# Kernel tuning notes

Measured on AMD Instinct MI355X. Metric: run time of the kernel, lower is better.

Reference implementation:

```python
import jax, jax.numpy as jnp
import numpy as np

B, L, H, NH = 4, 1024, 768, 12
HS = H // NH          # 64
DPB_DIM = H // 4      # 192
TEMPERATURE = 1.0


def setup_inputs() -> dict:
    key = jax.random.key(0)
    ks = jax.random.split(key, 10)
    def xavier(k, shape):
        fan_in, fan_out = shape[0], shape[-1]
        std = (2.0 / (fan_in + fan_out)) ** 0.5
        return jax.random.normal(k, shape, dtype=jnp.float32) * std
    return {
        "x": jax.random.normal(ks[0], (B, L, H), dtype=jnp.float32),
        "adj": jax.random.normal(ks[1], (B, 1, L, L), dtype=jnp.float32),
        "mask": jnp.ones((B, L), dtype=bool),
        "weights": xavier(ks[2], (H, 3 * H)),
        "in_bias": jnp.zeros((1, 1, 3 * H), dtype=jnp.float32),
        "out_bias": jnp.zeros((1, 1, H), dtype=jnp.float32),
        "dpb_w0": xavier(ks[3], (1, DPB_DIM)),
        "dpb_b0": jnp.zeros((DPB_DIM,), dtype=jnp.float32),
        "dpb_w1": xavier(ks[4], (DPB_DIM, DPB_DIM)),
        "dpb_b1": jnp.zeros((DPB_DIM,), dtype=jnp.float32),
        "dpb_w2": xavier(ks[5], (DPB_DIM, NH)),
        "dpb_b2": jnp.zeros((NH,), dtype=jnp.float32),
    }


def _dyn_pos_bias(n, w0, b0, w1, b1, w2, b2):
    # relative positions -(n-1)..(n-1) -> per-head bias [NH, n, n]
    pos = jnp.arange(-n + 1, n, dtype=jnp.float32)[:, None]      # [2n-1, 1]
    hdn = jax.nn.silu(pos @ w0 + b0)
    hdn = jax.nn.silu(hdn @ w1 + b1)
    table = hdn @ w2 + b2                                        # [2n-1, NH]
    idx = jnp.arange(n)[:, None] - jnp.arange(n)[None, :] + (n - 1)  # [n, n]
    return jnp.transpose(table[idx], (2, 0, 1))                  # [NH, n, n]


def reference(x, adj, mask, weights, in_bias, out_bias,
              dpb_w0, dpb_b0, dpb_w1, dpb_b1, dpb_w2, dpb_b2):
    b, l, h = x.shape
    qkv = x @ weights + in_bias                                  # [b, l, 3h]
    # view(b,l,NH,-1).permute(0,2,1,3).chunk(3, dim=3): split 3*HS per head
    qkv = jnp.transpose(qkv.reshape(b, l, NH, 3 * HS), (0, 2, 1, 3))  # [b,NH,l,3HS]
    Q, K, V = qkv[..., :HS], qkv[..., HS:2 * HS], qkv[..., 2 * HS:]
    norm = HS ** 0.5
    attention = jnp.einsum('bhid,bhjd->bhij', Q, K) / TEMPERATURE / norm
    raw_attention = attention                                    # returned pre-bias
    attn_bias = _dyn_pos_bias(l, dpb_w0, dpb_b0, dpb_w1, dpb_b1, dpb_w2, dpb_b2)
    attention = attention + attn_bias[None] + adj
    mask_value = -jnp.finfo(attention.dtype).max
    attention = jnp.where(mask[:, None, None, :], attention, mask_value)
    attention = jax.nn.softmax(attention, axis=-1)
    out = attention @ V                                          # [b,NH,l,HS]
    out = jnp.transpose(out, (0, 2, 1, 3)).reshape(b, l, h)
    out = out + out_bias
    return (out, raw_attention)
```

## Files before the change

kernel.cpp:

```cpp
#include <hip/hip_runtime.h>
#include <stdint.h>
#include <stddef.h>


#define BB 4
#define LL 1024
#define NHH 12
#define HSS 64
#define HH 768
#define OUT_ELEMS (BB * LL * HH)
#define QKV_ELEMS (BB * NHH * LL * HSS)

typedef __attribute__((ext_vector_type(8))) short short8;
typedef __attribute__((ext_vector_type(4))) float f32x4;

__device__ __forceinline__ float bf2f(ushort u) {
    union { unsigned int i; float f; } v; v.i = ((unsigned int)u) << 16; return v.f;
}
__device__ __forceinline__ ushort f2bf(float f) {
    union { float f; unsigned int i; } v; v.f = f;
    unsigned int r = v.i + 0x7FFFu + ((v.i >> 16) & 1u);
    return (ushort)(r >> 16);
}

__global__ void sentinel_kernel(float* out) {
    if (threadIdx.x == 0) out[0] = 12345.0f;
}

__global__ void dpb_kernel(const float* __restrict__ w0, const float* __restrict__ b0,
                           const float* __restrict__ w1, const float* __restrict__ b1,
                           const float* __restrict__ w2, const float* __restrict__ b2,
                           float* __restrict__ table) {
    __shared__ float h0s[192];
    __shared__ float h1s[192];
    int r = blockIdx.x, j = threadIdx.x;
    double pos = (double)(r - 1023);
    double a = pos * (double)w0[j] + (double)b0[j];
    h0s[j] = (float)(a / (1.0 + exp(-a)));
    __syncthreads();
    double acc = (double)b1[j];
    for (int k = 0; k < 192; ++k) acc += (double)h0s[k] * (double)w1[k * 192 + j];
    h1s[j] = (float)(acc / (1.0 + exp(-acc)));
    __syncthreads();
    if (j < 12) {
        double t = (double)b2[j];
        for (int k = 0; k < 192; ++k) t += (double)h1s[k] * (double)w2[k * 12 + j];
        table[r * 12 + j] = (float)t;
    }
}

__global__ __launch_bounds__(256)
void qkv_mfma(const float* __restrict__ x, const float* __restrict__ w,
              const float* __restrict__ bias,
              ushort* __restrict__ Qb, ushort* __restrict__ Kb, ushort* __restrict__ Vb) {
    __shared__ ushort As[64][32];
    __shared__ ushort Bts[64][56];

    int m0 = blockIdx.y * 64, n0 = blockIdx.x * 64;
    int tid = threadIdx.x, lane = tid & 63, wid = tid >> 6;
    int wr = wid >> 1, wc = wid & 1;
    int g = lane >> 4, qi = lane & 15;
    f32x4 acc[2][2] = {};

    int arow = tid >> 2, acol = (tid & 3) * 8;
    int bn = tid & 63, bkb = (tid >> 6) * 8;

    for (int k0 = 0; k0 < 768; k0 += 32) {
        float4 a0 = *(const float4*)(x + (size_t)(m0 + arow) * 768 + k0 + acol);
        float4 a1 = *(const float4*)(x + (size_t)(m0 + arow) * 768 + k0 + acol + 4);
        float bt[8];
        #pragma unroll
        for (int i = 0; i < 8; ++i)
            bt[i] = w[(size_t)(k0 + bkb + i) * 2304 + n0 + bn];
        short8 av, bv;
        av[0] = (short)f2bf(a0.x); av[1] = (short)f2bf(a0.y);
        av[2] = (short)f2bf(a0.z); av[3] = (short)f2bf(a0.w);
        av[4] = (short)f2bf(a1.x); av[5] = (short)f2bf(a1.y);
        av[6] = (short)f2bf(a1.z); av[7] = (short)f2bf(a1.w);
        #pragma unroll
        for (int i = 0; i < 8; ++i) bv[i] = (short)f2bf(bt[i]);
        *(short8*)&As[arow][acol] = av;
        *(short8*)&Bts[bn][bkb] = bv;
        __syncthreads();

        short8 af0 = *(const short8*)&As[wr * 32 + qi][g * 8];
        short8 af1 = *(const short8*)&As[wr * 32 + 16 + qi][g * 8];
        short8 bf0 = *(const short8*)&Bts[wc * 32 + qi][g * 8];
        short8 bf1 = *(const short8*)&Bts[wc * 32 + 16 + qi][g * 8];
        acc[0][0] = __builtin_amdgcn_mfma_f32_16x16x32_bf16(af0, bf0, acc[0][0], 0, 0, 0);
        acc[0][1] = __builtin_amdgcn_mfma_f32_16x16x32_bf16(af0, bf1, acc[0][1], 0, 0, 0);
        acc[1][0] = __builtin_amdgcn_mfma_f32_16x16x32_bf16(af1, bf0, acc[1][0], 0, 0, 0);
        acc[1][1] = __builtin_amdgcn_mfma_f32_16x16x32_bf16(af1, bf1, acc[1][1], 0, 0, 0);
        __syncthreads();
    }

    #pragma unroll
    for (int ti = 0; ti < 2; ++ti)
    #pragma unroll
    for (int tj = 0; tj < 2; ++tj)
    #pragma unroll
    for (int r = 0; r < 4; ++r) {
        int row = m0 + wr * 32 + ti * 16 + g * 4 + r;
        int col = n0 + wc * 32 + tj * 16 + qi;
        float val = acc[ti][tj][r] + bias[col];
        int h = col / 192, rem = col % 192;
        int which = rem >> 6, d = rem & 63;
        int bb = row >> 10, ll = row & 1023;
        ushort* dst = which == 0 ? Qb : (which == 1 ? Kb : Vb);
        dst[(((size_t)(bb * 12 + h) * 1024 + ll) << 6) + d] = f2bf(val);
    }
}

__global__ __launch_bounds__(256)
void attn_mfma(const ushort* __restrict__ Qb, const ushort* __restrict__ Kb,
               const ushort* __restrict__ Vb, const float* __restrict__ adj,
               const float* __restrict__ table,
               ushort* __restrict__ Opart, float* __restrict__ MZ,
               float* __restrict__ raw) {
    __shared__ ushort Ks[64][72];
    __shared__ ushort Vt[64][72];
    __shared__ ushort Ps[4][16][72];
    __shared__ float  tbl[576];

    int blk = blockIdx.x;
    int lb = (blk & 7) * 192 + (blk >> 3);
    int bh = lb >> 5;
    int rest = lb & 31;
    int half = rest >> 4;
    int qb = rest & 15;
    int h = bh % 12;
    int b = bh / 12;
    int q0 = qb * 64;
    int j_start = half * 512;
    int tid = threadIdx.x, lane = tid & 63, wid = tid >> 6;
    int g = lane >> 4, qi = lane & 15;
    int qg = q0 + wid * 16 + qi;
    int qrel = wid * 16 + qi;

    int tbase = q0 - j_start + 512;
    for (int i = tid; i < 575; i += 256) tbl[i] = table[(tbase + i) * 12 + h];

    short8 qfrag[2];
    qfrag[0] = *(const short8*)(Qb + ((size_t)(bh * 1024 + qg) << 6) + g * 8);
    qfrag[1] = *(const short8*)(Qb + ((size_t)(bh * 1024 + qg) << 6) + 32 + g * 8);

    float m = -INFINITY, ssum = 0.f;
    f32x4 oacc[4] = {};

    int krow = tid >> 2, kcol = (tid & 3) * 16;
    int vd = tid & 63, vjb = (tid >> 6) * 16;

    short8 kr0, kr1, vr0, vr1;
    {
        const ushort* kp = Kb + ((size_t)(bh * 1024 + j_start + krow) << 6) + kcol;
        kr0 = *(const short8*)kp;
        kr1 = *(const short8*)(kp + 8);
        ushort tmp[16];
        #pragma unroll
        for (int i = 0; i < 16; ++i)
            tmp[i] = Vb[((size_t)(bh * 1024 + j_start + vjb + i) << 6) + vd];
        #pragma unroll
        for (int i = 0; i < 8; ++i) { vr0[i] = (short)tmp[i]; vr1[i] = (short)tmp[i + 8]; }
    }

    for (int it = 0; it < 8; ++it) {
        int j0 = j_start + it * 64;
        *(short8*)&Ks[krow][kcol] = kr0;
        *(short8*)&Ks[krow][kcol + 8] = kr1;
        *(short8*)&Vt[vd][vjb] = vr0;
        *(short8*)&Vt[vd][vjb + 8] = vr1;
        __syncthreads();

        if (it < 7) {
            int jn = j0 + 64;
            const ushort* kp = Kb + ((size_t)(bh * 1024 + jn + krow) << 6) + kcol;
            kr0 = *(const short8*)kp;
            kr1 = *(const short8*)(kp + 8);
            ushort tmp[16];
            #pragma unroll
            for (int i = 0; i < 16; ++i)
                tmp[i] = Vb[((size_t)(bh * 1024 + jn + vjb + i) << 6) + vd];
            #pragma unroll
            for (int i = 0; i < 8; ++i) { vr0[i] = (short)tmp[i]; vr1[i] = (short)tmp[i + 8]; }
        }

        f32x4 sacc[4];
        #pragma unroll
        for (int jt = 0; jt < 4; ++jt) {
            short8 kf0 = *(const short8*)&Ks[jt * 16 + qi][g * 8];
            short8 kf1 = *(const short8*)&Ks[jt * 16 + qi][32 + g * 8];
            f32x4 z = {0.f, 0.f, 0.f, 0.f};
            z = __builtin_amdgcn_mfma_f32_16x16x32_bf16(kf0, qfrag[0], z, 0, 0, 0);
            z = __builtin_amdgcn_mfma_f32_16x16x32_bf16(kf1, qfrag[1], z, 0, 0, 0);
            sacc[jt] = z;
        }

        float lg[16];
        #pragma unroll
        for (int jt = 0; jt < 4; ++jt) {
            int jbase = j0 + jt * 16 + g * 4;
            f32x4 sv = sacc[jt] * 0.125f;
            *(f32x4*)(raw + ((size_t)(bh * 1024 + qg) << 10) + jbase) = sv;
            float4 av = *(const float4*)(adj + ((size_t)(b * 1024 + qg) << 10) + jbase);
            int ib = qrel + j_start + 511 - jbase;
            lg[jt * 4 + 0] = sv[0] + tbl[ib] + av.x;
            lg[jt * 4 + 1] = sv[1] + tbl[ib - 1] + av.y;
            lg[jt * 4 + 2] = sv[2] + tbl[ib - 2] + av.z;
            lg[jt * 4 + 3] = sv[3] + tbl[ib - 3] + av.w;
        }

        float cmax = lg[0];
        #pragma unroll
        for (int i = 1; i < 16; ++i) cmax = fmaxf(cmax, lg[i]);
        cmax = fmaxf(cmax, __shfl_xor(cmax, 16));
        cmax = fmaxf(cmax, __shfl_xor(cmax, 32));
        float newm = fmaxf(m, cmax);
        float corr = __expf(m - newm);
        float p[16], csum = 0.f;
        #pragma unroll
        for (int i = 0; i < 16; ++i) { p[i] = __expf(lg[i] - newm); csum += p[i]; }
        csum += __shfl_xor(csum, 16);
        csum += __shfl_xor(csum, 32);
        ssum = ssum * corr + csum;
        m = newm;
        #pragma unroll
        for (int dt = 0; dt < 4; ++dt) oacc[dt] *= corr;

        #pragma unroll
        for (int jt = 0; jt < 4; ++jt) {
            ushort4 pw;
            #pragma unroll
            for (int r = 0; r < 4; ++r) ((ushort*)&pw)[r] = f2bf(p[jt * 4 + r]);
            *(ushort4*)&Ps[wid][qi][jt * 16 + g * 4] = pw;
        }
        short8 pf0 = *(const short8*)&Ps[wid][qi][g * 8];
        short8 pf1 = *(const short8*)&Ps[wid][qi][32 + g * 8];
        #pragma unroll
        for (int dt = 0; dt < 4; ++dt) {
            short8 vf0 = *(const short8*)&Vt[dt * 16 + qi][g * 8];
            short8 vf1 = *(const short8*)&Vt[dt * 16 + qi][32 + g * 8];
            oacc[dt] = __builtin_amdgcn_mfma_f32_16x16x32_bf16(vf0, pf0, oacc[dt], 0, 0, 0);
            oacc[dt] = __builtin_amdgcn_mfma_f32_16x16x32_bf16(vf1, pf1, oacc[dt], 0, 0, 0);
        }
        __syncthreads();
    }

    int pb = (bh * 16 + qb) * 2 + half;
    #pragma unroll
    for (int dt = 0; dt < 4; ++dt) {
        ushort4 ow;
        #pragma unroll
        for (int r = 0; r < 4; ++r) ((ushort*)&ow)[r] = f2bf(oacc[dt][r]);
        *(ushort4*)(Opart + (size_t)pb * 4096 + qrel * 64 + dt * 16 + g * 4) = ow;
    }
    if (g == 0) {
        MZ[pb * 128 + qrel * 2] = m;
        MZ[pb * 128 + qrel * 2 + 1] = ssum;
    }
}

__global__ __launch_bounds__(256)
void combine_kernel(const ushort* __restrict__ Opart, const float* __restrict__ MZ,
                    const float* __restrict__ out_bias, float* __restrict__ out) {
    int cb = blockIdx.x;
    int bh = cb >> 4, qb = cb & 15;
    int h = bh % 12, b = bh / 12;
    int t = threadIdx.x;
    int q = t >> 2, dg = (t & 3) * 16;
    int p0 = cb * 2, p1 = p0 + 1;
    float m0 = MZ[p0 * 128 + q * 2], Z0 = MZ[p0 * 128 + q * 2 + 1];
    float m1 = MZ[p1 * 128 + q * 2], Z1 = MZ[p1 * 128 + q * 2 + 1];
    float mm = fmaxf(m0, m1);
    float a0 = __expf(m0 - mm), a1 = __expf(m1 - mm);
    float inv = 1.f / (a0 * Z0 + a1 * Z1);
    const ushort* r0 = Opart + (size_t)p0 * 4096 + q * 64 + dg;
    const ushort* r1 = Opart + (size_t)p1 * 4096 + q * 64 + dg;
    short8 x0a = *(const short8*)r0, x0b = *(const short8*)(r0 + 8);
    short8 x1a = *(const short8*)r1, x1b = *(const short8*)(r1 + 8);
    float* op = out + (size_t)(b * 1024 + qb * 64 + q) * 768 + h * 64 + dg;
    const float* ob = out_bias + h * 64 + dg;
    float res[16];
    #pragma unroll
    for (int i = 0; i < 8; ++i) {
        res[i]     = (a0 * bf2f((ushort)x0a[i]) + a1 * bf2f((ushort)x1a[i])) * inv + ob[i];
        res[i + 8] = (a0 * bf2f((ushort)x0b[i]) + a1 * bf2f((ushort)x1b[i])) * inv + ob[i + 8];
    }
    #pragma unroll
    for (int i = 0; i < 4; ++i)
        *(float4*)(op + i * 4) = *(float4*)(res + i * 4);
}

extern "C" void kernel_launch(void* const* d_in, const int* in_sizes, int n_in,
                              void* d_out, int out_size, void* d_ws, size_t ws_size,
                              hipStream_t stream) {
    const float* x        = (const float*)d_in[0];
    const float* adj      = (const float*)d_in[1];
    const float* weights  = (const float*)d_in[3];
    const float* in_bias  = (const float*)d_in[4];
    const float* out_bias = (const float*)d_in[5];
    const float* dpb_w0   = (const float*)d_in[6];
    const float* dpb_b0   = (const float*)d_in[7];
    const float* dpb_w1   = (const float*)d_in[8];
    const float* dpb_b1   = (const float*)d_in[9];
    const float* dpb_w2   = (const float*)d_in[10];
    const float* dpb_b2   = (const float*)d_in[11];

    float* out = (float*)d_out;
    float* raw = out + OUT_ELEMS;

    float*  table = (float*)d_ws;
    ushort* Qb    = (ushort*)((char*)d_ws + 98304);
    ushort* Kb    = Qb + QKV_ELEMS;
    ushort* Vb    = Kb + QKV_ELEMS;
    ushort* Opart = Vb + QKV_ELEMS;
    float*  MZ    = (float*)(Opart + (size_t)1536 * 4096);
    size_t need = 98304 + 3 * (size_t)QKV_ELEMS * 2
                + (size_t)1536 * 4096 * 2 + (size_t)1536 * 128 * 4;
    if (ws_size < need) {
        sentinel_kernel<<<1, 64, 0, stream>>>(out);
        return;
    }

    dpb_kernel<<<2047, 192, 0, stream>>>(dpb_w0, dpb_b0, dpb_w1, dpb_b1, dpb_w2, dpb_b2, table);
    qkv_mfma<<<dim3(2304 / 64, 4096 / 64), 256, 0, stream>>>(x, weights, in_bias, Qb, Kb, Vb);
    attn_mfma<<<1536, 256, 0, stream>>>(Qb, Kb, Vb, adj, table, Opart, MZ, raw);
    combine_kernel<<<768, 256, 0, stream>>>(Opart, MZ, out_bias, out);
}
```

Baseline: 147.7 us.

## Pre-convert QKV inputs to bf16, pipeline GEMM loads, prefetch adj in attention

```diff
diff --git a/kernel.cpp b/kernel.cpp
--- a/kernel.cpp
+++ b/kernel.cpp
@@ -10,6 +10,8 @@
 #define HH 768
 #define OUT_ELEMS (BB * LL * HH)
 #define QKV_ELEMS (BB * NHH * LL * HSS)
+#define X_ELEMS (BB * LL * HH)
+#define W_ELEMS (HH * 3 * HH)
 
 typedef __attribute__((ext_vector_type(8))) short short8;
 typedef __attribute__((ext_vector_type(4))) float f32x4;
@@ -25,6 +27,20 @@
 
 __global__ void sentinel_kernel(float* out) {
     if (threadIdx.x == 0) out[0] = 12345.0f;
+}
+
+__global__ __launch_bounds__(256)
+void cvt_bf16(const float* __restrict__ src, ushort* __restrict__ dst, int n) {
+    int i = (blockIdx.x * 256 + threadIdx.x) * 8;
+    if (i >= n) return;
+    float4 a = *(const float4*)(src + i);
+    float4 b = *(const float4*)(src + i + 4);
+    short8 o;
+    o[0] = (short)f2bf(a.x); o[1] = (short)f2bf(a.y);
+    o[2] = (short)f2bf(a.z); o[3] = (short)f2bf(a.w);
+    o[4] = (short)f2bf(b.x); o[5] = (short)f2bf(b.y);
+    o[6] = (short)f2bf(b.z); o[7] = (short)f2bf(b.w);
+    *(short8*)(dst + i) = o;
 }
 
 __global__ void dpb_kernel(const float* __restrict__ w0, const float* __restrict__ b0,
@@ -50,11 +66,11 @@
 }
 
 __global__ __launch_bounds__(256)
-void qkv_mfma(const float* __restrict__ x, const float* __restrict__ w,
+void qkv_mfma(const ushort* __restrict__ x, const ushort* __restrict__ w,
               const float* __restrict__ bias,
               ushort* __restrict__ Qb, ushort* __restrict__ Kb, ushort* __restrict__ Vb) {
-    __shared__ ushort As[64][32];
-    __shared__ ushort Bts[64][56];
+    __shared__ ushort As[64][72];
+    __shared__ ushort Bts[64][72];
 
     int m0 = blockIdx.y * 64, n0 = blockIdx.x * 64;
     int tid = threadIdx.x, lane = tid & 63, wid = tid >> 6;
@@ -62,35 +78,55 @@
     int g = lane >> 4, qi = lane & 15;
     f32x4 acc[2][2] = {};
 
-    int arow = tid >> 2, acol = (tid & 3) * 8;
-    int bn = tid & 63, bkb = (tid >> 6) * 8;
-
-    for (int k0 = 0; k0 < 768; k0 += 32) {
-        float4 a0 = *(const float4*)(x + (size_t)(m0 + arow) * 768 + k0 + acol);
-        float4 a1 = *(const float4*)(x + (size_t)(m0 + arow) * 768 + k0 + acol + 4);
-        float bt[8];
-        #pragma unroll
-        for (int i = 0; i < 8; ++i)
-            bt[i] = w[(size_t)(k0 + bkb + i) * 2304 + n0 + bn];
-        short8 av, bv;
-        av[0] = (short)f2bf(a0.x); av[1] = (short)f2bf(a0.y);
-        av[2] = (short)f2bf(a0.z); av[3] = (short)f2bf(a0.w);
-        av[4] = (short)f2bf(a1.x); av[5] = (short)f2bf(a1.y);
-        av[6] = (short)f2bf(a1.z); av[7] = (short)f2bf(a1.w);
-        #pragma unroll
-        for (int i = 0; i < 8; ++i) bv[i] = (short)f2bf(bt[i]);
-        *(short8*)&As[arow][acol] = av;
-        *(short8*)&Bts[bn][bkb] = bv;
+    int arow = tid >> 2, acol = (tid & 3) * 16;
+    int bn = tid & 63, bkb = (tid >> 6) * 16;
+
+    const size_t xrow = (size_t)(m0 + arow) * 768;
+    short8 ar0, ar1, br0, br1;
+
+    {
+        ar0 = *(const short8*)(x + xrow + acol);
+        ar1 = *(const short8*)(x + xrow + acol + 8);
+        ushort t[16];
+        #pragma unroll
+        for (int i = 0; i < 16; ++i)
+            t[i] = w[(size_t)(bkb + i) * 2304 + n0 + bn];
+        #pragma unroll
+        for (int i = 0; i < 8; ++i) { br0[i] = (short)t[i]; br1[i] = (short)t[i + 8]; }
+    }
+
+    for (int kt = 0; kt < 12; ++kt) {
+        *(short8*)&As[arow][acol] = ar0;
+        *(short8*)&As[arow][acol + 8] = ar1;
+        *(short8*)&Bts[bn][bkb] = br0;
+        *(short8*)&Bts[bn][bkb + 8] = br1;
         __syncthreads();
 
-        short8 af0 = *(const short8*)&As[wr * 32 + qi][g * 8];
-        short8 af1 = *(const short8*)&As[wr * 32 + 16 + qi][g * 8];
-        short8 bf0 = *(const short8*)&Bts[wc * 32 + qi][g * 8];
-        short8 bf1 = *(const short8*)&Bts[wc * 32 + 16 + qi][g * 8];
-        acc[0][0] = __builtin_amdgcn_mfma_f32_16x16x32_bf16(af0, bf0, acc[0][0], 0, 0, 0);
-        acc[0][1] = __builtin_amdgcn_mfma_f32_16x16x32_bf16(af0, bf1, acc[0][1], 0, 0, 0);
-        acc[1][0] = __builtin_amdgcn_mfma_f32_16x16x32_bf16(af1, bf0, acc[1][0], 0, 0, 0);
-        acc[1][1] = __builtin_amdgcn_mfma_f32_16x16x32_bf16(af1, bf1, acc[1][1], 0, 0, 0);
+        if (kt < 11) {
+            int k0 = kt * 64 + 64;
+            ar0 = *(const short8*)(x + xrow + k0 + acol);
+            ar1 = *(const short8*)(x + xrow + k0 + acol + 8);
+            ushort t[16];
+            #pragma unroll
+            for (int i = 0; i < 16; ++i)
+                t[i] = w[(size_t)(k0 + bkb + i) * 2304 + n0 + bn];
+            #pragma unroll
+            for (int i = 0; i < 8; ++i) { br0[i] = (short)t[i]; br1[i] = (short)t[i + 8]; }
+        }
+
+        __builtin_amdgcn_s_setprio(1);
+        #pragma unroll
+        for (int kk = 0; kk < 64; kk += 32) {
+            short8 af0 = *(const short8*)&As[wr * 32 + qi][kk + g * 8];
+            short8 af1 = *(const short8*)&As[wr * 32 + 16 + qi][kk + g * 8];
+            short8 bf0 = *(const short8*)&Bts[wc * 32 + qi][kk + g * 8];
+            short8 bf1 = *(const short8*)&Bts[wc * 32 + 16 + qi][kk + g * 8];
+            acc[0][0] = __builtin_amdgcn_mfma_f32_16x16x32_bf16(af0, bf0, acc[0][0], 0, 0, 0);
+            acc[0][1] = __builtin_amdgcn_mfma_f32_16x16x32_bf16(af0, bf1, acc[0][1], 0, 0, 0);
+            acc[1][0] = __builtin_amdgcn_mfma_f32_16x16x32_bf16(af1, bf0, acc[1][0], 0, 0, 0);
+            acc[1][1] = __builtin_amdgcn_mfma_f32_16x16x32_bf16(af1, bf1, acc[1][1], 0, 0, 0);
+        }
+        __builtin_amdgcn_s_setprio(0);
         __syncthreads();
     }
 
@@ -111,7 +147,7 @@
     }
 }
 
-__global__ __launch_bounds__(256)
+__global__ __launch_bounds__(256, 5)
 void attn_mfma(const ushort* __restrict__ Qb, const ushort* __restrict__ Kb,
                const ushort* __restrict__ Vb, const float* __restrict__ adj,
                const float* __restrict__ table,
@@ -150,7 +186,10 @@
     int krow = tid >> 2, kcol = (tid & 3) * 16;
     int vd = tid & 63, vjb = (tid >> 6) * 16;
 
+    const float* adjrow = adj + ((size_t)(b * 1024 + qg) << 10);
+
     short8 kr0, kr1, vr0, vr1;
+    float4 acur[4], anxt[4];
     {
         const ushort* kp = Kb + ((size_t)(bh * 1024 + j_start + krow) << 6) + kcol;
         kr0 = *(const short8*)kp;
@@ -161,6 +200,9 @@
             tmp[i] = Vb[((size_t)(bh * 1024 + j_start + vjb + i) << 6) + vd];
         #pragma unroll
         for (int i = 0; i < 8; ++i) { vr0[i] = (short)tmp[i]; vr1[i] = (short)tmp[i + 8]; }
+        #pragma unroll
+        for (int jt = 0; jt < 4; ++jt)
+            acur[jt] = *(const float4*)(adjrow + j_start + jt * 16 + g * 4);
     }
 
     for (int it = 0; it < 8; ++it) {
@@ -182,9 +224,13 @@
                 tmp[i] = Vb[((size_t)(bh * 1024 + jn + vjb + i) << 6) + vd];
             #pragma unroll
             for (int i = 0; i < 8; ++i) { vr0[i] = (short)tmp[i]; vr1[i] = (short)tmp[i + 8]; }
+            #pragma unroll
+            for (int jt = 0; jt < 4; ++jt)
+                anxt[jt] = *(const float4*)(adjrow + jn + jt * 16 + g * 4);
         }
 
         f32x4 sacc[4];
+        __builtin_amdgcn_s_setprio(1);
         #pragma unroll
         for (int jt = 0; jt < 4; ++jt) {
             short8 kf0 = *(const short8*)&Ks[jt * 16 + qi][g * 8];
@@ -194,6 +240,7 @@
             z = __builtin_amdgcn_mfma_f32_16x16x32_bf16(kf1, qfrag[1], z, 0, 0, 0);
             sacc[jt] = z;
         }
+        __builtin_amdgcn_s_setprio(0);
 
         float lg[16];
         #pragma unroll
@@ -201,12 +248,11 @@
             int jbase = j0 + jt * 16 + g * 4;
             f32x4 sv = sacc[jt] * 0.125f;
             *(f32x4*)(raw + ((size_t)(bh * 1024 + qg) << 10) + jbase) = sv;
-            float4 av = *(const float4*)(adj + ((size_t)(b * 1024 + qg) << 10) + jbase);
             int ib = qrel + j_start + 511 - jbase;
-            lg[jt * 4 + 0] = sv[0] + tbl[ib] + av.x;
-            lg[jt * 4 + 1] = sv[1] + tbl[ib - 1] + av.y;
-            lg[jt * 4 + 2] = sv[2] + tbl[ib - 2] + av.z;
-            lg[jt * 4 + 3] = sv[3] + tbl[ib - 3] + av.w;
+            lg[jt * 4 + 0] = sv[0] + tbl[ib] + acur[jt].x;
+            lg[jt * 4 + 1] = sv[1] + tbl[ib - 1] + acur[jt].y;
+            lg[jt * 4 + 2] = sv[2] + tbl[ib - 2] + acur[jt].z;
+            lg[jt * 4 + 3] = sv[3] + tbl[ib - 3] + acur[jt].w;
         }
 
         float cmax = lg[0];
@@ -235,6 +281,7 @@
         }
         short8 pf0 = *(const short8*)&Ps[wid][qi][g * 8];
         short8 pf1 = *(const short8*)&Ps[wid][qi][32 + g * 8];
+        __builtin_amdgcn_s_setprio(1);
         #pragma unroll
         for (int dt = 0; dt < 4; ++dt) {
             short8 vf0 = *(const short8*)&Vt[dt * 16 + qi][g * 8];
@@ -242,7 +289,11 @@
             oacc[dt] = __builtin_amdgcn_mfma_f32_16x16x32_bf16(vf0, pf0, oacc[dt], 0, 0, 0);
             oacc[dt] = __builtin_amdgcn_mfma_f32_16x16x32_bf16(vf1, pf1, oacc[dt], 0, 0, 0);
         }
+        __builtin_amdgcn_s_setprio(0);
         __syncthreads();
+
+        #pragma unroll
+        for (int jt = 0; jt < 4; ++jt) acur[jt] = anxt[jt];
     }
 
     int pb = (bh * 16 + qb) * 2 + half;
@@ -308,21 +359,26 @@
     float* out = (float*)d_out;
     float* raw = out + OUT_ELEMS;
 
-    float*  table = (float*)d_ws;
-    ushort* Qb    = (ushort*)((char*)d_ws + 98304);
-    ushort* Kb    = Qb + QKV_ELEMS;
-    ushort* Vb    = Kb + QKV_ELEMS;
-    ushort* Opart = Vb + QKV_ELEMS;
-    float*  MZ    = (float*)(Opart + (size_t)1536 * 4096);
-    size_t need = 98304 + 3 * (size_t)QKV_ELEMS * 2
-                + (size_t)1536 * 4096 * 2 + (size_t)1536 * 128 * 4;
+    char* base = (char*)d_ws;
+    float*  table  = (float*)base;
+    char*   shared = base + 98304;
+    ushort* xb     = (ushort*)shared;
+    ushort* wb     = xb + X_ELEMS;
+    ushort* Opart  = (ushort*)shared;
+    float*  MZ     = (float*)(shared + 12582912);
+    ushort* Qb     = (ushort*)(shared + 13369344);
+    ushort* Kb     = Qb + QKV_ELEMS;
+    ushort* Vb     = Kb + QKV_ELEMS;
+    size_t need = 98304 + 13369344 + 3 * (size_t)QKV_ELEMS * 2;
     if (ws_size < need) {
         sentinel_kernel<<<1, 64, 0, stream>>>(out);
         return;
     }
 
+    cvt_bf16<<<X_ELEMS / (256 * 8), 256, 0, stream>>>(x, xb, X_ELEMS);
+    cvt_bf16<<<W_ELEMS / (256 * 8), 256, 0, stream>>>(weights, wb, W_ELEMS);
     dpb_kernel<<<2047, 192, 0, stream>>>(dpb_w0, dpb_b0, dpb_w1, dpb_b1, dpb_w2, dpb_b2, table);
-    qkv_mfma<<<dim3(2304 / 64, 4096 / 64), 256, 0, stream>>>(x, weights, in_bias, Qb, Kb, Vb);
+    qkv_mfma<<<dim3(2304 / 64, 4096 / 64), 256, 0, stream>>>(xb, wb, in_bias, Qb, Kb, Vb);
     attn_mfma<<<1536, 256, 0, stream>>>(Qb, Kb, Vb, adj, table, Opart, MZ, raw);
     combine_kernel<<<768, 256, 0, stream>>>(Opart, MZ, out_bias, out);
 }
```

New measurement: 209.8 us, median of 3. 42.0% more time.
